# Performance work log

Hardware: AMD Instinct MI355X
Metric: run time of the kernel (lower is better)

Reference implementation:

```python
import jax, jax.numpy as jnp
import numpy as np

EMBED = 1024
ATTN = 1024

def setup_inputs() -> dict:
    key = jax.random.key(0)
    k1, k2, k3, k4 = jax.random.split(key, 4)
    x = jax.random.normal(k1, (32, 2048, EMBED), dtype=jnp.float32)
    W = jax.random.normal(k2, (EMBED, ATTN), dtype=jnp.float32) / np.sqrt(EMBED)
    b = jax.random.normal(k3, (ATTN,), dtype=jnp.float32) * 0.01
    ctx = jax.random.normal(k4, (ATTN,), dtype=jnp.float32)
    return {"x": x, "W": W, "b": b, "ctx": ctx}

def reference(x, W, b, ctx):
    # scores: [B, S] = tanh(x @ W + b) . ctx
    h = jnp.tanh(jnp.einsum('bse,ea->bsa', x, W) + b)
    scores = jnp.einsum('bsa,a->bs', h, ctx)
    weights = jax.nn.softmax(scores, axis=1)            # softmax over seq dim
    return jnp.einsum('bse,bs->be', x, weights)          # weighted sum pooling
```

## Files before the change

### kernel.cpp

```cpp
#include <hip/hip_runtime.h>
#include <hip/hip_bf16.h>

typedef _Float16 half8 __attribute__((ext_vector_type(8)));
typedef _Float16 half4 __attribute__((ext_vector_type(4)));
typedef float floatx4 __attribute__((ext_vector_type(4)));

#define EMBED 1024
#define SEQ   2048
#define BATCH 32
#define M_TOT (BATCH * SEQ)
#define KDIM  1024
#define NDIM  1024

#define GLOAD16(g, l) __builtin_amdgcn_global_load_lds(                      \
    (const __attribute__((address_space(1))) void*)(g),                      \
    (__attribute__((address_space(3))) void*)(l), 16, 0, 0)

__global__ void transpose_w_kernel(const float* __restrict__ W,
                                   _Float16* __restrict__ Wt) {
    __shared__ float t[32][33];
    const int kt = blockIdx.x * 32;
    const int nt = blockIdx.y * 32;
    #pragma unroll
    for (int i = 0; i < 4; ++i)
        t[threadIdx.y + 8 * i][threadIdx.x] =
            W[(size_t)(kt + threadIdx.y + 8 * i) * NDIM + nt + threadIdx.x];
    __syncthreads();
    #pragma unroll
    for (int i = 0; i < 4; ++i)
        Wt[(size_t)(nt + threadIdx.y + 8 * i) * KDIM + kt + threadIdx.x] =
            (_Float16)t[threadIdx.x][threadIdx.y + 8 * i];
}

__global__ void zero_kernel(float* __restrict__ scores, float* __restrict__ out) {
    const int i = blockIdx.x * 256 + threadIdx.x;
    if (i < M_TOT) scores[i] = 0.0f;
    if (i < BATCH * EMBED) out[i] = 0.0f;
}

__global__ __launch_bounds__(256) void cvt_x_kernel(const float* __restrict__ x,
                                                    _Float16* __restrict__ x16) {
    const size_t stride = (size_t)gridDim.x * 256 * 8;
    for (size_t i = ((size_t)blockIdx.x * 256 + threadIdx.x) * 8;
         i < (size_t)M_TOT * KDIM; i += stride) {
        const float4 a = *(const float4*)(x + i);
        const float4 b = *(const float4*)(x + i + 4);
        half8 h;
        h[0] = (_Float16)a.x; h[1] = (_Float16)a.y; h[2] = (_Float16)a.z; h[3] = (_Float16)a.w;
        h[4] = (_Float16)b.x; h[5] = (_Float16)b.y; h[6] = (_Float16)b.z; h[7] = (_Float16)b.w;
        *(half8*)(x16 + i) = h;
    }
}

__global__ __launch_bounds__(256, 3) void score_gemm7(
    const _Float16* __restrict__ x16, const _Float16* __restrict__ Wt,
    const float* __restrict__ bias, const float* __restrict__ ctx,
    float* __restrict__ scores) {
    __shared__ _Float16 As[3][128 * 32];
    __shared__ _Float16 Bs[3][128 * 32];

    const int nb = ((blockIdx.x & 7) << 9) | (blockIdx.x >> 3);
    const int bm = nb >> 3;
    const int bn = nb & 7;
    const int tid = threadIdx.x;
    const int lane = tid & 63;
    const int wid = tid >> 6;
    const int wm = wid >> 1;
    const int wn = wid & 1;

    const int jA0 = wid * 2;
    const int lrow = lane >> 2;
    const int gslot = (lane & 3) ^ (lrow & 3);
    const int gcol = gslot * 8;

    const _Float16* Ab = x16 + (size_t)(bm * 128) * KDIM;
    const _Float16* Bb = Wt  + (size_t)(bn * 128) * KDIM;

    floatx4 acc[4][4] = {};

    const int fslot = ((lane >> 4) ^ (lane & 3)) * 8;
    const int frow = lane & 15;

    #define STAGE(buf, kt)                                                        \
        {                                                                         \
            const int kc = (kt) * 32 + gcol;                                      \
            _Pragma("unroll")                                                     \
            for (int i = 0; i < 2; ++i) {                                         \
                const int j = jA0 + i;                                            \
                GLOAD16(Ab + (size_t)(j * 16 + lrow) * KDIM + kc, &As[buf][j * 512]); \
                GLOAD16(Bb + (size_t)(j * 16 + lrow) * KDIM + kc, &Bs[buf][j * 512]); \
            }                                                                     \
        }

    #define COMPUTE(buf)                                                          \
        {                                                                         \
            half8 afr[4], bfr[4];                                                 \
            _Pragma("unroll")                                                     \
            for (int m = 0; m < 4; ++m)                                           \
                afr[m] = *(const half8*)&As[buf][(wm * 64 + m * 16 + frow) * 32 + fslot]; \
            _Pragma("unroll")                                                     \
            for (int n = 0; n < 4; ++n)                                           \
                bfr[n] = *(const half8*)&Bs[buf][(wn * 64 + n * 16 + frow) * 32 + fslot]; \
            __builtin_amdgcn_s_setprio(1);                                        \
            _Pragma("unroll")                                                     \
            for (int m = 0; m < 4; ++m)                                           \
                _Pragma("unroll")                                                 \
                for (int n = 0; n < 4; ++n)                                       \
                    acc[m][n] = __builtin_amdgcn_mfma_f32_16x16x32_f16(           \
                        afr[m], bfr[n], acc[m][n], 0, 0, 0);                      \
            __builtin_amdgcn_s_setprio(0);                                        \
        }

    STAGE(0, 0);
    STAGE(1, 1);

    int cur = 0;
    int stg = 2;
    for (int kt = 0; kt < KDIM / 32 - 2; ++kt) {
        STAGE(stg, kt + 2);
        asm volatile("s_waitcnt vmcnt(8)" ::: "memory");
        __builtin_amdgcn_s_barrier();
        COMPUTE(cur);
        __builtin_amdgcn_s_barrier();
        cur = (cur == 2) ? 0 : cur + 1;
        stg = (stg == 2) ? 0 : stg + 1;
    }
    asm volatile("s_waitcnt vmcnt(4)" ::: "memory");
    __builtin_amdgcn_s_barrier();
    COMPUTE(cur);
    __builtin_amdgcn_s_barrier();
    cur = (cur == 2) ? 0 : cur + 1;
    asm volatile("s_waitcnt vmcnt(0)" ::: "memory");
    __builtin_amdgcn_s_barrier();
    COMPUTE(cur);

    #undef COMPUTE
    #undef STAGE

    float bv[4], cv[4];
    #pragma unroll
    for (int n = 0; n < 4; ++n) {
        const int col = bn * 128 + wn * 64 + n * 16 + (lane & 15);
        bv[n] = bias[col];
        cv[n] = ctx[col];
    }
    #pragma unroll
    for (int m = 0; m < 4; ++m) {
        #pragma unroll
        for (int j = 0; j < 4; ++j) {
            float partial = 0.0f;
            #pragma unroll
            for (int n = 0; n < 4; ++n) {
                const float v = acc[m][n][j] + bv[n];
                const float e = __expf(2.0f * v);
                const float t = 1.0f - 2.0f * __builtin_amdgcn_rcpf(e + 1.0f);
                partial += t * cv[n];
            }
            #pragma unroll
            for (int off = 1; off < 16; off <<= 1)
                partial += __shfl_xor(partial, off, 64);
            if ((lane & 15) == 0) {
                const int rowg = bm * 128 + wm * 64 + m * 16 + (lane >> 4) * 4 + j;
                atomicAdd(&scores[rowg], partial);
            }
        }
    }
}

__global__ __launch_bounds__(256) void score_gemm_f32(
    const float* __restrict__ A32p, const _Float16* __restrict__ Wt,
    const float* __restrict__ bias, const float* __restrict__ ctx,
    float* __restrict__ scores) {
    __shared__ _Float16 As[128 * 64];
    __shared__ _Float16 Bs[128 * 64];

    const int bid = blockIdx.x;
    const int bm = bid >> 3;
    const int bn = bid & 7;
    const int tid = threadIdx.x;
    const int lane = tid & 63;
    const int wid = tid >> 6;
    const int wm = wid >> 1;
    const int wn = wid & 1;

    const int c = tid & 7;
    const int r0 = tid >> 3;
    const int swz = (r0 & 7) << 3;
    const int wcol = (c * 8) ^ swz;

    float4 aF[4][2];
    int4   bR[4];

    #pragma unroll
    for (int i = 0; i < 4; ++i) {
        const int row = r0 + 32 * i;
        const float* p = A32p + (size_t)(bm * 128 + row) * KDIM + c * 8;
        aF[i][0] = *(const float4*)p;
        aF[i][1] = *(const float4*)(p + 4);
        bR[i] = *(const int4*)(Wt + (size_t)(bn * 128 + row) * KDIM + c * 8);
    }

    floatx4 acc[4][4] = {};

    for (int kt = 0; kt < KDIM / 64; ++kt) {
        __syncthreads();
        #pragma unroll
        for (int i = 0; i < 4; ++i) {
            const int row = r0 + 32 * i;
            half8 h;
            h[0] = (_Float16)aF[i][0].x; h[1] = (_Float16)aF[i][0].y;
            h[2] = (_Float16)aF[i][0].z; h[3] = (_Float16)aF[i][0].w;
            h[4] = (_Float16)aF[i][1].x; h[5] = (_Float16)aF[i][1].y;
            h[6] = (_Float16)aF[i][1].z; h[7] = (_Float16)aF[i][1].w;
            *(half8*)&As[row * 64 + wcol] = h;
            *(int4*)&Bs[row * 64 + wcol] = bR[i];
        }
        __syncthreads();

        if (kt + 1 < KDIM / 64) {
            #pragma unroll
            for (int i = 0; i < 4; ++i) {
                const int row = r0 + 32 * i;
                const float* p = A32p + (size_t)(bm * 128 + row) * KDIM + (kt + 1) * 64 + c * 8;
                aF[i][0] = *(const float4*)p;
                aF[i][1] = *(const float4*)(p + 4);
                bR[i] = *(const int4*)(Wt + (size_t)(bn * 128 + row) * KDIM + (kt + 1) * 64 + c * 8);
            }
        }

        #pragma unroll
        for (int s = 0; s < 2; ++s) {
            half8 afr[4], bfr[4];
            const int colr = s * 32 + (lane >> 4) * 8;
            #pragma unroll
            for (int m = 0; m < 4; ++m) {
                const int row = wm * 64 + m * 16 + (lane & 15);
                afr[m] = *(const half8*)&As[row * 64 + (colr ^ ((row & 7) << 3))];
            }
            #pragma unroll
            for (int n = 0; n < 4; ++n) {
                const int row = wn * 64 + n * 16 + (lane & 15);
                bfr[n] = *(const half8*)&Bs[row * 64 + (colr ^ ((row & 7) << 3))];
            }
            #pragma unroll
            for (int m = 0; m < 4; ++m)
                #pragma unroll
                for (int n = 0; n < 4; ++n)
                    acc[m][n] = __builtin_amdgcn_mfma_f32_16x16x32_f16(
                        afr[m], bfr[n], acc[m][n], 0, 0, 0);
        }
    }

    float bv[4], cv[4];
    #pragma unroll
    for (int n = 0; n < 4; ++n) {
        const int col = bn * 128 + wn * 64 + n * 16 + (lane & 15);
        bv[n] = bias[col];
        cv[n] = ctx[col];
    }
    #pragma unroll
    for (int m = 0; m < 4; ++m) {
        #pragma unroll
        for (int j = 0; j < 4; ++j) {
            float partial = 0.0f;
            #pragma unroll
            for (int n = 0; n < 4; ++n) {
                const float v = acc[m][n][j] + bv[n];
                const float e = __expf(2.0f * v);
                const float t = 1.0f - 2.0f * __builtin_amdgcn_rcpf(e + 1.0f);
                partial += t * cv[n];
            }
            #pragma unroll
            for (int off = 1; off < 16; off <<= 1)
                partial += __shfl_xor(partial, off, 64);
            if ((lane & 15) == 0) {
                const int rowg = bm * 128 + wm * 64 + m * 16 + (lane >> 4) * 4 + j;
                atomicAdd(&scores[rowg], partial);
            }
        }
    }
}

__global__ void softmax_kernel(const float* __restrict__ scores,
                               float* __restrict__ weights) {
    const int bb = blockIdx.x;
    const int tid = threadIdx.x;
    const float* s = scores + (size_t)bb * SEQ;
    float* w = weights + (size_t)bb * SEQ;

    __shared__ float red[8];

    float v[8];
    float mx = -1e30f;
    #pragma unroll
    for (int i = 0; i < 8; ++i) {
        v[i] = s[tid + i * 256];
        mx = fmaxf(mx, v[i]);
    }
    #pragma unroll
    for (int off = 1; off < 64; off <<= 1)
        mx = fmaxf(mx, __shfl_xor(mx, off, 64));
    const int wv = tid >> 6;
    if ((tid & 63) == 0) red[wv] = mx;
    __syncthreads();
    mx = fmaxf(fmaxf(red[0], red[1]), fmaxf(red[2], red[3]));

    float sum = 0.0f;
    #pragma unroll
    for (int i = 0; i < 8; ++i) {
        v[i] = __expf(v[i] - mx);
        sum += v[i];
    }
    #pragma unroll
    for (int off = 1; off < 64; off <<= 1)
        sum += __shfl_xor(sum, off, 64);
    if ((tid & 63) == 0) red[4 + wv] = sum;
    __syncthreads();
    sum = red[4] + red[5] + red[6] + red[7];
    const float inv = 1.0f / sum;
    #pragma unroll
    for (int i = 0; i < 8; ++i)
        w[tid + i * 256] = v[i] * inv;
}

__global__ __launch_bounds__(256) void pool_kernel(const float* __restrict__ x,
                                                   const float* __restrict__ weights,
                                                   float* __restrict__ out) {
    const int bb = blockIdx.x >> 4;
    const int sc = blockIdx.x & 15;
    const int tid = threadIdx.x;

    const float4* xb = (const float4*)(x + (size_t)bb * SEQ * EMBED) +
                       (size_t)(sc * 128) * (EMBED / 4) + tid;
    const float* wb = weights + (size_t)bb * SEQ + sc * 128;

    float ax = 0.f, ay = 0.f, az = 0.f, aw = 0.f;
    #pragma unroll 4
    for (int s = 0; s < 128; ++s) {
        const float wgt = wb[s];
        const float4 xv = xb[(size_t)s * (EMBED / 4)];
        ax += wgt * xv.x; ay += wgt * xv.y; az += wgt * xv.z; aw += wgt * xv.w;
    }
    float* o = out + (size_t)bb * EMBED + tid * 4;
    atomicAdd(o + 0, ax);
    atomicAdd(o + 1, ay);
    atomicAdd(o + 2, az);
    atomicAdd(o + 3, aw);
}

__global__ __launch_bounds__(256) void pool16_kernel(const _Float16* __restrict__ x16,
                                                     const float* __restrict__ weights,
                                                     float* __restrict__ out) {
    const int bb = blockIdx.x >> 4;
    const int sc = blockIdx.x & 15;
    const int tid = threadIdx.x;

    const _Float16* xb = x16 + (size_t)bb * SEQ * EMBED +
                         (size_t)(sc * 128) * EMBED + tid * 4;
    const float* wb = weights + (size_t)bb * SEQ + sc * 128;

    float ax = 0.f, ay = 0.f, az = 0.f, aw = 0.f;
    #pragma unroll 4
    for (int s = 0; s < 128; ++s) {
        const float wgt = wb[s];
        const half4 h = *(const half4*)(xb + (size_t)s * EMBED);
        ax += wgt * (float)h[0]; ay += wgt * (float)h[1];
        az += wgt * (float)h[2]; aw += wgt * (float)h[3];
    }
    float* o = out + (size_t)bb * EMBED + tid * 4;
    atomicAdd(o + 0, ax);
    atomicAdd(o + 1, ay);
    atomicAdd(o + 2, az);
    atomicAdd(o + 3, aw);
}

extern "C" void kernel_launch(void* const* d_in, const int* in_sizes, int n_in,
                              void* d_out, int out_size, void* d_ws, size_t ws_size,
                              hipStream_t stream) {
    const float* x   = (const float*)d_in[0];
    const float* W   = (const float*)d_in[1];
    const float* b   = (const float*)d_in[2];
    const float* ctx = (const float*)d_in[3];
    float* out = (float*)d_out;

    char* ws = (char*)d_ws;
    _Float16* Wt      = (_Float16*)ws;
    float*    scores  = (float*)(ws + (2u << 20));
    float*    weights = (float*)(ws + (2u << 20) + (256u << 10));
    _Float16* x16     = (_Float16*)(ws + (4u << 20));

    const size_t need = (4ull << 20) + ((size_t)M_TOT * KDIM * 2);
    const bool fast = ws_size >= need;

    hipLaunchKernelGGL(transpose_w_kernel, dim3(32, 32), dim3(32, 8), 0, stream, W, Wt);
    hipLaunchKernelGGL(zero_kernel, dim3(M_TOT / 256), dim3(256), 0, stream, scores, out);

    if (fast) {
        hipLaunchKernelGGL(cvt_x_kernel, dim3(4096), dim3(256), 0, stream, x, x16);
        hipLaunchKernelGGL(score_gemm7, dim3(4096), dim3(256), 0, stream,
                           x16, Wt, b, ctx, scores);
    } else {
        hipLaunchKernelGGL(score_gemm_f32, dim3(4096), dim3(256), 0, stream,
                           x, Wt, b, ctx, scores);
    }

    hipLaunchKernelGGL(softmax_kernel, dim3(BATCH), dim3(256), 0, stream, scores, weights);

    if (fast) {
        hipLaunchKernelGGL(pool16_kernel, dim3(BATCH * 16), dim3(256), 0, stream,
                           x16, weights, out);
    } else {
        hipLaunchKernelGGL(pool_kernel, dim3(BATCH * 16), dim3(256), 0, stream,
                           x, weights, out);
    }
}
```

Measured before the change: 306.6 us.

## Enlarge score GEMM tile to 256x128 with 8 waves and double buffering

The score GEMM now uses 512-thread blocks computing 256x128 output tiles with 8 waves, halving the grid. The LDS ring drops from triple to double buffering with a new swizzle, and s_setprio hints are removed in favour of sched_barrier. The larger M tile means each B tile loaded into shared memory is reused across more rows, which cuts global traffic per FLOP. The trade-off is shallower prefetch depth, which may expose load latency, plus more LDS per block and possible occupancy limits.

```diff
diff --git a/kernel.cpp b/kernel.cpp
--- a/kernel.cpp
+++ b/kernel.cpp
@@ -52,44 +52,43 @@
     }
 }
 
-__global__ __launch_bounds__(256, 3) void score_gemm7(
+__global__ __launch_bounds__(512, 4) void score_gemm14(
     const _Float16* __restrict__ x16, const _Float16* __restrict__ Wt,
     const float* __restrict__ bias, const float* __restrict__ ctx,
     float* __restrict__ scores) {
-    __shared__ _Float16 As[3][128 * 32];
-    __shared__ _Float16 Bs[3][128 * 32];
-
-    const int nb = ((blockIdx.x & 7) << 9) | (blockIdx.x >> 3);
+    __shared__ _Float16 As[2][256 * 32];
+    __shared__ _Float16 Bs[2][128 * 32];
+
+    const int nb = ((blockIdx.x & 7) << 8) | (blockIdx.x >> 3);
     const int bm = nb >> 3;
     const int bn = nb & 7;
     const int tid = threadIdx.x;
     const int lane = tid & 63;
-    const int wid = tid >> 6;
-    const int wm = wid >> 1;
-    const int wn = wid & 1;
-
-    const int jA0 = wid * 2;
+    const int w = tid >> 6;
+    const int wm = w >> 1;
+    const int wn = w & 1;
+
     const int lrow = lane >> 2;
-    const int gslot = (lane & 3) ^ (lrow & 3);
+    const int gslot = (lane & 3) ^ ((lane >> 3) & 3);
     const int gcol = gslot * 8;
 
-    const _Float16* Ab = x16 + (size_t)(bm * 128) * KDIM;
+    const _Float16* Ab = x16 + (size_t)(bm * 256) * KDIM;
     const _Float16* Bb = Wt  + (size_t)(bn * 128) * KDIM;
 
     floatx4 acc[4][4] = {};
 
-    const int fslot = ((lane >> 4) ^ (lane & 3)) * 8;
     const int frow = lane & 15;
+    const int fslot = ((lane >> 4) ^ ((frow >> 1) & 3)) * 8;
 
     #define STAGE(buf, kt)                                                        \
         {                                                                         \
             const int kc = (kt) * 32 + gcol;                                      \
             _Pragma("unroll")                                                     \
             for (int i = 0; i < 2; ++i) {                                         \
-                const int j = jA0 + i;                                            \
+                const int j = w + i * 8;                                          \
                 GLOAD16(Ab + (size_t)(j * 16 + lrow) * KDIM + kc, &As[buf][j * 512]); \
-                GLOAD16(Bb + (size_t)(j * 16 + lrow) * KDIM + kc, &Bs[buf][j * 512]); \
             }                                                                     \
+            GLOAD16(Bb + (size_t)(w * 16 + lrow) * KDIM + kc, &Bs[buf][w * 512]); \
         }
 
     #define COMPUTE(buf)                                                          \
@@ -101,38 +100,29 @@
             _Pragma("unroll")                                                     \
             for (int n = 0; n < 4; ++n)                                           \
                 bfr[n] = *(const half8*)&Bs[buf][(wn * 64 + n * 16 + frow) * 32 + fslot]; \
-            __builtin_amdgcn_s_setprio(1);                                        \
             _Pragma("unroll")                                                     \
             for (int m = 0; m < 4; ++m)                                           \
                 _Pragma("unroll")                                                 \
                 for (int n = 0; n < 4; ++n)                                       \
                     acc[m][n] = __builtin_amdgcn_mfma_f32_16x16x32_f16(           \
                         afr[m], bfr[n], acc[m][n], 0, 0, 0);                      \
-            __builtin_amdgcn_s_setprio(0);                                        \
         }
 
     STAGE(0, 0);
-    STAGE(1, 1);
-
-    int cur = 0;
-    int stg = 2;
-    for (int kt = 0; kt < KDIM / 32 - 2; ++kt) {
-        STAGE(stg, kt + 2);
-        asm volatile("s_waitcnt vmcnt(8)" ::: "memory");
+
+    for (int kt = 0; kt < 31; ++kt) {
+        const int cur = kt & 1;
+        STAGE(cur ^ 1, kt + 1);
+        asm volatile("s_waitcnt vmcnt(3)" ::: "memory");
+        __builtin_amdgcn_sched_barrier(0);
         __builtin_amdgcn_s_barrier();
         COMPUTE(cur);
         __builtin_amdgcn_s_barrier();
-        cur = (cur == 2) ? 0 : cur + 1;
-        stg = (stg == 2) ? 0 : stg + 1;
-    }
-    asm volatile("s_waitcnt vmcnt(4)" ::: "memory");
+    }
+    asm volatile("s_waitcnt vmcnt(0)" ::: "memory");
+    __builtin_amdgcn_sched_barrier(0);
     __builtin_amdgcn_s_barrier();
-    COMPUTE(cur);
-    __builtin_amdgcn_s_barrier();
-    cur = (cur == 2) ? 0 : cur + 1;
-    asm volatile("s_waitcnt vmcnt(0)" ::: "memory");
-    __builtin_amdgcn_s_barrier();
-    COMPUTE(cur);
+    COMPUTE(1);
 
     #undef COMPUTE
     #undef STAGE
@@ -140,7 +130,7 @@
     float bv[4], cv[4];
     #pragma unroll
     for (int n = 0; n < 4; ++n) {
-        const int col = bn * 128 + wn * 64 + n * 16 + (lane & 15);
+        const int col = bn * 128 + wn * 64 + n * 16 + frow;
         bv[n] = bias[col];
         cv[n] = ctx[col];
     }
@@ -159,8 +149,8 @@
             #pragma unroll
             for (int off = 1; off < 16; off <<= 1)
                 partial += __shfl_xor(partial, off, 64);
-            if ((lane & 15) == 0) {
-                const int rowg = bm * 128 + wm * 64 + m * 16 + (lane >> 4) * 4 + j;
+            if (frow == 0) {
+                const int rowg = bm * 256 + wm * 64 + m * 16 + (lane >> 4) * 4 + j;
                 atomicAdd(&scores[rowg], partial);
             }
         }
@@ -392,12 +382,12 @@
     const size_t need = (4ull << 20) + ((size_t)M_TOT * KDIM * 2);
     const bool fast = ws_size >= need;
 
+    hipLaunchKernelGGL(zero_kernel, dim3(M_TOT / 256), dim3(256), 0, stream, scores, out);
     hipLaunchKernelGGL(transpose_w_kernel, dim3(32, 32), dim3(32, 8), 0, stream, W, Wt);
-    hipLaunchKernelGGL(zero_kernel, dim3(M_TOT / 256), dim3(256), 0, stream, scores, out);
 
     if (fast) {
         hipLaunchKernelGGL(cvt_x_kernel, dim3(4096), dim3(256), 0, stream, x, x16);
-        hipLaunchKernelGGL(score_gemm7, dim3(4096), dim3(256), 0, stream,
+        hipLaunchKernelGGL(score_gemm14, dim3(2048), dim3(512), 0, stream,
                            x16, Wt, b, ctx, scores);
     } else {
         hipLaunchKernelGGL(score_gemm_f32, dim3(4096), dim3(256), 0, stream,
```

After: 284.6 us, median of 3. 1.08x faster.

## Deepen GEMM LDS pipeline to four stages with new swizzle and occupancy bound

Applied to the files above, without the earlier changes.

Raises the score GEMM's shared-memory ring from three to four buffers, so three K-tiles are in flight instead of two, and adjusts the vmcnt waits to match. The tail iterations are unrolled with constant buffer indices, and sched_barriers are added so the compiler cannot reorder work across the waits. The LDS XOR swizzle pattern is changed, likely to cut bank conflicts on the fragment reads, and launch bounds drop from 3 to 2 blocks per CU, which reflects the larger LDS footprint and loosens register limits. Lower occupancy may offset the gain from deeper prefetch.

```diff
diff --git a/kernel.cpp b/kernel.cpp
--- a/kernel.cpp
+++ b/kernel.cpp
@@ -52,12 +52,12 @@
     }
 }
 
-__global__ __launch_bounds__(256, 3) void score_gemm7(
+__global__ __launch_bounds__(256, 2) void score_gemm15(
     const _Float16* __restrict__ x16, const _Float16* __restrict__ Wt,
     const float* __restrict__ bias, const float* __restrict__ ctx,
     float* __restrict__ scores) {
-    __shared__ _Float16 As[3][128 * 32];
-    __shared__ _Float16 Bs[3][128 * 32];
+    __shared__ _Float16 As[4][128 * 32];
+    __shared__ _Float16 Bs[4][128 * 32];
 
     const int nb = ((blockIdx.x & 7) << 9) | (blockIdx.x >> 3);
     const int bm = nb >> 3;
@@ -70,7 +70,7 @@
 
     const int jA0 = wid * 2;
     const int lrow = lane >> 2;
-    const int gslot = (lane & 3) ^ (lrow & 3);
+    const int gslot = (lane & 3) ^ ((lane >> 3) & 3);
     const int gcol = gslot * 8;
 
     const _Float16* Ab = x16 + (size_t)(bm * 128) * KDIM;
@@ -78,8 +78,8 @@
 
     floatx4 acc[4][4] = {};
 
-    const int fslot = ((lane >> 4) ^ (lane & 3)) * 8;
     const int frow = lane & 15;
+    const int fslot = ((lane >> 4) ^ ((frow >> 1) & 3)) * 8;
 
     #define STAGE(buf, kt)                                                        \
         {                                                                         \
@@ -113,26 +113,30 @@
 
     STAGE(0, 0);
     STAGE(1, 1);
-
-    int cur = 0;
-    int stg = 2;
-    for (int kt = 0; kt < KDIM / 32 - 2; ++kt) {
-        STAGE(stg, kt + 2);
-        asm volatile("s_waitcnt vmcnt(8)" ::: "memory");
+    STAGE(2, 2);
+
+    for (int kt = 0; kt < 29; ++kt) {
+        STAGE((kt + 3) & 3, kt + 3);
+        asm volatile("s_waitcnt vmcnt(12)" ::: "memory");
+        __builtin_amdgcn_sched_barrier(0);
         __builtin_amdgcn_s_barrier();
-        COMPUTE(cur);
+        COMPUTE(kt & 3);
         __builtin_amdgcn_s_barrier();
-        cur = (cur == 2) ? 0 : cur + 1;
-        stg = (stg == 2) ? 0 : stg + 1;
-    }
+    }
+    asm volatile("s_waitcnt vmcnt(8)" ::: "memory");
+    __builtin_amdgcn_sched_barrier(0);
+    __builtin_amdgcn_s_barrier();
+    COMPUTE(1);
+    __builtin_amdgcn_s_barrier();
     asm volatile("s_waitcnt vmcnt(4)" ::: "memory");
+    __builtin_amdgcn_sched_barrier(0);
     __builtin_amdgcn_s_barrier();
-    COMPUTE(cur);
+    COMPUTE(2);
     __builtin_amdgcn_s_barrier();
-    cur = (cur == 2) ? 0 : cur + 1;
     asm volatile("s_waitcnt vmcnt(0)" ::: "memory");
+    __builtin_amdgcn_sched_barrier(0);
     __builtin_amdgcn_s_barrier();
-    COMPUTE(cur);
+    COMPUTE(3);
 
     #undef COMPUTE
     #undef STAGE
@@ -392,12 +396,12 @@
     const size_t need = (4ull << 20) + ((size_t)M_TOT * KDIM * 2);
     const bool fast = ws_size >= need;
 
+    hipLaunchKernelGGL(zero_kernel, dim3(M_TOT / 256), dim3(256), 0, stream, scores, out);
     hipLaunchKernelGGL(transpose_w_kernel, dim3(32, 32), dim3(32, 8), 0, stream, W, Wt);
-    hipLaunchKernelGGL(zero_kernel, dim3(M_TOT / 256), dim3(256), 0, stream, scores, out);
 
     if (fast) {
         hipLaunchKernelGGL(cvt_x_kernel, dim3(4096), dim3(256), 0, stream, x, x16);
-        hipLaunchKernelGGL(score_gemm7, dim3(4096), dim3(256), 0, stream,
+        hipLaunchKernelGGL(score_gemm15, dim3(4096), dim3(256), 0, stream,
                            x16, Wt, b, ctx, scores);
     } else {
         hipLaunchKernelGGL(score_gemm_f32, dim3(4096), dim3(256), 0, stream,
```

Result: slower. 353.7 us (+15.4%).
